# Kernel tuning notes

Hardware: AMD Instinct MI355X
Metric: run time of the kernel (lower is better)

Reference implementation:

```python
import jax, jax.numpy as jnp
import numpy as np

T, D, F, E, TOPK = 4096, 2048, 4096, 8, 2


def setup_inputs() -> dict:
    key = jax.random.key(0)
    ks = jax.random.split(key, 5)
    scale = 0.02
    return {
        "x": jax.random.normal(ks[0], (T, D), dtype=jnp.float32),
        "gate_w": jax.random.normal(ks[1], (D, E), dtype=jnp.float32) * scale,
        "w1": jax.random.normal(ks[2], (E, D, F), dtype=jnp.float32) * scale,
        "w3": jax.random.normal(ks[3], (E, D, F), dtype=jnp.float32) * scale,
        "w2": jax.random.normal(ks[4], (E, F, D), dtype=jnp.float32) * scale,
    }


def reference(x, gate_w, w1, w3, w2):
    # --- top-k gating (matches torch.topk + softmax over selected logits) ---
    gate_logits = x @ gate_w                                   # [T, E]
    top_w, sel = jax.lax.top_k(gate_logits, TOPK)              # [T, K]
    top_w = jax.nn.softmax(top_w.astype(jnp.float32), axis=1).astype(x.dtype)
    # combine weights scattered to dense [T, E]; 0 for unselected experts
    t_idx = jnp.arange(x.shape[0])[:, None]                    # [T, 1]
    cw = jnp.zeros(gate_logits.shape, x.dtype).at[t_idx, sel].add(top_w)  # [T, E]

    # --- all experts as batched GEMMs (SwiGLU FFN), combined by gate weights ---
    h = jnp.einsum('td,edf->etf', x, w1)                       # [E, T, F]
    g = jnp.einsum('td,edf->etf', x, w3)                       # [E, T, F]
    expert_out = jnp.einsum('etf,efd->etd', jax.nn.silu(h) * g, w2)  # [E, T, D]
    return jnp.einsum('te,etd->td', cw, expert_out)            # [T, D]
```

## Files before the change

### kernel.cpp

```cpp
#include <hip/hip_runtime.h>
#include <hip/hip_bf16.h>

#define T_TOK 4096
#define DDIM  2048
#define FDIM  4096
#define NEXP  8
#define MAXROWS 9216
#define MAXMT   72
#define G1_GRID (MAXMT * 64)
#define CV2_GRID 16384
#define FUSED_GRID (512 * 41)

typedef __attribute__((ext_vector_type(4))) float f32x4;
typedef __attribute__((ext_vector_type(8))) short bf16x8;

__device__ __forceinline__ unsigned short f2b(float f) {
  union { float f; unsigned u; } c; c.f = f;
  unsigned r = c.u + 0x7FFFu + ((c.u >> 16) & 1u);
  return (unsigned short)(r >> 16);
}

__device__ __forceinline__ void gload_lds16(const void* g, void* l) {
  __builtin_amdgcn_global_load_lds((__attribute__((address_space(1))) void*)(g),
                                   (__attribute__((address_space(3))) void*)(l),
                                   16, 0, 0);
}

__device__ __forceinline__ void xcd_map2d(int bid, int MT_PER, int NT, int& mt, int& nt) {
  const int xcd = bid & 7;
  const int li = bid >> 3;
  const int grp = MT_PER * 4;
  const int ng = li / grp;
  const int rem = li % grp;
  mt = xcd * MT_PER + (rem >> 2);
  nt = ng * 4 + (rem & 3);
}

__global__ void gate_topk(const float* __restrict__ x, const float* __restrict__ gw,
                          int* __restrict__ sel_e, float* __restrict__ sel_w) {
  const int t = blockIdx.x * 4 + (threadIdx.x >> 6);
  const int l = threadIdx.x & 63;
  const float* xr = x + (size_t)t * DDIM;
  float acc[8];
  #pragma unroll
  for (int e = 0; e < 8; ++e) acc[e] = 0.f;
  for (int d = l; d < DDIM; d += 64) {
    const float xv = xr[d];
    const float* g = gw + d * 8;
    #pragma unroll
    for (int e = 0; e < 8; ++e) acc[e] = fmaf(xv, g[e], acc[e]);
  }
  #pragma unroll
  for (int e = 0; e < 8; ++e) {
    float v = acc[e];
    #pragma unroll
    for (int off = 32; off; off >>= 1) v += __shfl_xor(v, off, 64);
    acc[e] = v;
  }
  if (l == 0) {
    int e0 = 0; float v0 = acc[0];
    #pragma unroll
    for (int e = 1; e < 8; ++e) if (acc[e] > v0) { v0 = acc[e]; e0 = e; }
    int e1 = -1; float v1 = -1e30f;
    #pragma unroll
    for (int e = 0; e < 8; ++e) if (e != e0 && acc[e] > v1) { v1 = acc[e]; e1 = e; }
    const float ex = __expf(v1 - v0);
    const float w0 = 1.f / (1.f + ex);
    sel_e[t * 2] = e0; sel_e[t * 2 + 1] = e1;
    sel_w[t * 2] = w0; sel_w[t * 2 + 1] = ex * w0;
  }
}

__global__ void build_lists(const int* __restrict__ sel_e, const float* __restrict__ sel_w,
                            int* __restrict__ cnt, int* __restrict__ base,
                            int* __restrict__ row_token, float* __restrict__ row_gw,
                            int* __restrict__ trow) {
  __shared__ int c[8], f[8], b[9];
  const int tid = threadIdx.x;
  if (tid < 8) { c[tid] = 0; f[tid] = 0; }
  __syncthreads();
  for (int t = tid; t < T_TOK; t += 256) {
    atomicAdd(&c[sel_e[t * 2]], 1);
    atomicAdd(&c[sel_e[t * 2 + 1]], 1);
  }
  __syncthreads();
  if (tid == 0) {
    int r = 0;
    for (int e = 0; e < 8; ++e) { b[e] = r; r += ((c[e] + 127) >> 7) << 7; }
    b[8] = r;
    for (int e = 0; e < 8; ++e) { cnt[e] = c[e]; base[e] = b[e]; }
    base[8] = r;
  }
  __syncthreads();
  for (int i = tid; i < MAXROWS; i += 256) { row_token[i] = -1; row_gw[i] = 0.f; }
  __syncthreads();
  for (int t = tid; t < T_TOK; t += 256) {
    #pragma unroll
    for (int k = 0; k < 2; ++k) {
      const int e = sel_e[t * 2 + k];
      const int p = b[e] + atomicAdd(&f[e], 1);
      row_token[p] = t; row_gw[p] = sel_w[t * 2 + k];
      trow[t * 2 + k] = p;
    }
  }
}

__global__ void gather_x(const float* __restrict__ x, const int* __restrict__ base,
                         const int* __restrict__ row_token, unsigned short* __restrict__ xc) {
  const int i = blockIdx.x;
  if (i >= base[8]) return;
  const int t = row_token[i];
  const int tid = threadIdx.x;
  union { uint4 u; unsigned short s[8]; } o;
  if (t < 0) { o.u.x = 0u; o.u.y = 0u; o.u.z = 0u; o.u.w = 0u; }
  else {
    const float4* src = (const float4*)(x + (size_t)t * DDIM + tid * 8);
    const float4 a = src[0], bb = src[1];
    o.s[0] = f2b(a.x);  o.s[1] = f2b(a.y);  o.s[2] = f2b(a.z);  o.s[3] = f2b(a.w);
    o.s[4] = f2b(bb.x); o.s[5] = f2b(bb.y); o.s[6] = f2b(bb.z); o.s[7] = f2b(bb.w);
  }
  ((uint4*)(xc + (size_t)i * DDIM))[tid] = o.u;
}

__device__ __forceinline__ void conv_tile(const float* s, unsigned short* d,
                                          int R, int C, int rowMul, int rowAdd,
                                          int r0, int c0, int tid,
                                          unsigned short (*T)[68]) {
  {
    const int i = tid >> 2, jb = (tid & 3) * 16;
    #pragma unroll
    for (int k2 = 0; k2 < 4; ++k2) {
      const float4 v = *(const float4*)(s + (size_t)(r0 + i) * C + c0 + jb + k2 * 4);
      uint2 uu;
      uu.x = (unsigned)f2b(v.x) | ((unsigned)f2b(v.y) << 16);
      uu.y = (unsigned)f2b(v.z) | ((unsigned)f2b(v.w) << 16);
      *(uint2*)&T[i][jb + k2 * 4] = uu;
    }
  }
  __syncthreads();
  {
    const int j = tid >> 2, ib = (tid & 3) * 16;
    union { uint4 q[2]; unsigned short s16[16]; } pk;
    #pragma unroll
    for (int i = 0; i < 16; ++i) pk.s16[i] = T[ib + i][j];
    unsigned short* drow = d + (size_t)(rowMul * (c0 + j) + rowAdd) * R + r0 + ib;
    *(uint4*)drow = pk.q[0];
    *(uint4*)(drow + 8) = pk.q[1];
  }
}

__global__ void conv_w13(const float* __restrict__ w1, const float* __restrict__ w3,
                         unsigned short* __restrict__ dst) {
  __shared__ unsigned short T[64][68];
  const int z = blockIdx.z;
  const int e = z & 7;
  const int isw3 = z >> 3;
  const float* s = (isw3 ? w3 : w1) + (size_t)e * DDIM * FDIM;
  unsigned short* d = dst + (size_t)e * DDIM * FDIM * 2;
  conv_tile(s, d, DDIM, FDIM, 2, isw3, blockIdx.x * 64, blockIdx.y * 64, threadIdx.x, T);
}

__global__ void conv_w2(const float* __restrict__ w2, unsigned short* __restrict__ dst) {
  __shared__ unsigned short T[64][68];
  const int e = blockIdx.z;
  const float* s = w2 + (size_t)e * FDIM * DDIM;
  unsigned short* d = dst + (size_t)e * FDIM * DDIM;
  conv_tile(s, d, FDIM, DDIM, 1, 0, blockIdx.x * 64, blockIdx.y * 64, threadIdx.x, T);
}

__device__ __forceinline__ void gemm1_body(int bid,
                                           const unsigned short* __restrict__ A,
                                           const unsigned short* __restrict__ B,
                                           const int* __restrict__ base,
                                           unsigned short* __restrict__ hid,
                                           unsigned short* As, unsigned short* Bs) {
  constexpr int KDIM = DDIM;
  constexpr int NDIM = 2 * FDIM;

  int mt, nt;
  xcd_map2d(bid, MAXMT / 8, NDIM / 128, mt, nt);

  const int m0 = mt * 128;
  if (m0 >= base[8]) return;
  int e = 0;
  #pragma unroll
  for (int qq = 1; qq < 8; ++qq) if (m0 >= base[qq]) e = qq;
  const int n0 = nt * 128;
  const unsigned short* Bp = B + (size_t)e * NDIM * KDIM;

  const int tid = threadIdx.x;
  const int l = tid & 63;
  const int w = tid >> 6;
  const int wm = w >> 1, wn = w & 1;
  const int lr = l & 15, kc = l >> 4;

  const f32x4 vzero = {0.f, 0.f, 0.f, 0.f};
  f32x4 acc[4][4];
  #pragma unroll
  for (int i = 0; i < 4; ++i)
    #pragma unroll
    for (int j = 0; j < 4; ++j) acc[i][j] = vzero;

  const int srow = w * 32 + (l >> 3);
  const int sc = l & 7;
  const unsigned short* Arow = A + (size_t)(m0 + srow) * KDIM;
  const unsigned short* Brow = Bp + (size_t)(n0 + srow) * KDIM;

  for (int k0 = 0; k0 < KDIM; k0 += 64) {
    #pragma unroll
    for (int qq = 0; qq < 4; ++qq) {
      const int r = srow + qq * 8;
      const int cg = (sc ^ (r & 7)) << 3;
      gload_lds16(Arow + (size_t)qq * 8 * KDIM + k0 + cg, As + w * 2048 + qq * 512);
      gload_lds16(Brow + (size_t)qq * 8 * KDIM + k0 + cg, Bs + w * 2048 + qq * 512);
    }
    __syncthreads();
    #pragma unroll
    for (int ks = 0; ks < 2; ++ks) {
      bf16x8 af[4], bfr[4];
      #pragma unroll
      for (int mf = 0; mf < 4; ++mf) {
        const int r = wm * 64 + mf * 16 + lr;
        const int c = (ks * 4 + kc) ^ (r & 7);
        af[mf] = *(const bf16x8*)((const char*)As + r * 128 + c * 16);
      }
      #pragma unroll
      for (int nf = 0; nf < 4; ++nf) {
        const int n = wn * 64 + nf * 16 + lr;
        const int c = (ks * 4 + kc) ^ (n & 7);
        bfr[nf] = *(const bf16x8*)((const char*)Bs + n * 128 + c * 16);
      }
      #pragma unroll
      for (int mf = 0; mf < 4; ++mf)
        #pragma unroll
        for (int nf = 0; nf < 4; ++nf)
          acc[mf][nf] = __builtin_amdgcn_mfma_f32_16x16x32_bf16(af[mf], bfr[nf], acc[mf][nf], 0, 0, 0);
    }
    __syncthreads();
  }

  const int fbase = (n0 >> 1) + wn * 32;
  #pragma unroll
  for (int mf = 0; mf < 4; ++mf) {
    const int row = m0 + wm * 64 + mf * 16 + (kc << 2);
    #pragma unroll
    for (int nf = 0; nf < 4; ++nf)
      #pragma unroll
      for (int rr = 0; rr < 4; ++rr) {
        const float v = acc[mf][nf][rr];
        const float o = __shfl_xor(v, 1, 64);
        const float h = (l & 1) ? o : v;
        const float g = (l & 1) ? v : o;
        const float res = (h / (1.f + __expf(-h))) * g;
        const float vc = __shfl(res, (l & 48) | ((l & 7) << 1), 64);
        if (lr < 8)
          hid[(size_t)(row + rr) * FDIM + fbase + nf * 8 + (l & 7)] = f2b(vc);
      }
  }
}

__global__ void moe_gemm1(const unsigned short* __restrict__ A,
                          const unsigned short* __restrict__ B,
                          const int* __restrict__ base,
                          unsigned short* __restrict__ hid) {
  __shared__ __align__(16) unsigned short As[128 * 64];
  __shared__ __align__(16) unsigned short Bs[128 * 64];
  gemm1_body(blockIdx.x, A, B, base, hid, As, Bs);
}

__global__ void gemm1_fused(const unsigned short* __restrict__ A,
                            const unsigned short* __restrict__ B,
                            const int* __restrict__ base,
                            unsigned short* __restrict__ hid,
                            const float* __restrict__ w2,
                            unsigned short* __restrict__ w2t) {
  __shared__ __align__(16) unsigned short As[128 * 64];
  __shared__ __align__(16) unsigned short Bs[128 * 64];
  const int g = blockIdx.x / 41;
  const int r = blockIdx.x % 41;
  if (r < 9) {
    gemm1_body(g * 9 + r, A, B, base, hid, As, Bs);
  } else {
    const int cid = g * 32 + (r - 9);
    const int e = cid >> 11;
    const int rem = cid & 2047;
    const int r0 = (rem >> 5) * 64;
    const int c0 = (rem & 31) * 64;
    conv_tile(w2 + (size_t)e * FDIM * DDIM, w2t + (size_t)e * FDIM * DDIM,
              FDIM, DDIM, 1, 0, r0, c0, threadIdx.x, (unsigned short (*)[68])As);
  }
}

__global__ void moe_gemm2(const unsigned short* __restrict__ A,
                          const unsigned short* __restrict__ B,
                          const int* __restrict__ base,
                          unsigned short* __restrict__ eo) {
  constexpr int KDIM = FDIM;
  constexpr int NDIM = DDIM;

  int mt, ntl;
  xcd_map2d(blockIdx.x, MAXMT / 8, NDIM / 128, mt, ntl);

  const int m0 = mt * 128;
  if (m0 >= base[8]) return;
  int e = 0;
  #pragma unroll
  for (int qq = 1; qq < 8; ++qq) if (m0 >= base[qq]) e = qq;
  const int n0 = ntl * 128;
  const unsigned short* Bp = B + (size_t)e * NDIM * KDIM;

  __shared__ __align__(16) unsigned short As[128 * 64];
  __shared__ __align__(16) unsigned short Bs[128 * 64];

  const int tid = threadIdx.x;
  const int l = tid & 63;
  const int w = tid >> 6;
  const int wm = w >> 1, wn = w & 1;
  const int lr = l & 15, kc = l >> 4;

  const f32x4 vzero = {0.f, 0.f, 0.f, 0.f};
  f32x4 acc[4][4];
  #pragma unroll
  for (int i = 0; i < 4; ++i)
    #pragma unroll
    for (int j = 0; j < 4; ++j) acc[i][j] = vzero;

  const int srow = w * 32 + (l >> 3);
  const int sc = l & 7;
  const unsigned short* Arow = A + (size_t)(m0 + srow) * KDIM;
  const unsigned short* Brow = Bp + (size_t)(n0 + srow) * KDIM;

  for (int k0 = 0; k0 < KDIM; k0 += 64) {
    #pragma unroll
    for (int qq = 0; qq < 4; ++qq) {
      const int r = srow + qq * 8;
      const int cg = (sc ^ (r & 7)) << 3;
      gload_lds16(Arow + (size_t)qq * 8 * KDIM + k0 + cg,
                  (unsigned short*)As + w * 2048 + qq * 512);
      gload_lds16(Brow + (size_t)qq * 8 * KDIM + k0 + cg,
                  (unsigned short*)Bs + w * 2048 + qq * 512);
    }
    __syncthreads();
    #pragma unroll
    for (int ks = 0; ks < 2; ++ks) {
      bf16x8 af[4], bfr[4];
      #pragma unroll
      for (int mf = 0; mf < 4; ++mf) {
        const int r = wm * 64 + mf * 16 + lr;
        const int c = (ks * 4 + kc) ^ (r & 7);
        af[mf] = *(const bf16x8*)((const char*)As + r * 128 + c * 16);
      }
      #pragma unroll
      for (int nf = 0; nf < 4; ++nf) {
        const int n = wn * 64 + nf * 16 + lr;
        const int c = (ks * 4 + kc) ^ (n & 7);
        bfr[nf] = *(const bf16x8*)((const char*)Bs + n * 128 + c * 16);
      }
      #pragma unroll
      for (int mf = 0; mf < 4; ++mf)
        #pragma unroll
        for (int nf = 0; nf < 4; ++nf)
          acc[mf][nf] = __builtin_amdgcn_mfma_f32_16x16x32_bf16(af[mf], bfr[nf], acc[mf][nf], 0, 0, 0);
    }
    __syncthreads();
  }
  #pragma unroll
  for (int mf = 0; mf < 4; ++mf) {
    const int row = m0 + wm * 64 + mf * 16 + (kc << 2);
    #pragma unroll
    for (int rr = 0; rr < 4; ++rr) {
      unsigned short* erow = eo + (size_t)(row + rr) * DDIM;
      #pragma unroll
      for (int nf = 0; nf < 4; ++nf) {
        const int col = n0 + wn * 64 + nf * 16 + lr;
        erow[col] = f2b(acc[mf][nf][rr]);
      }
    }
  }
}

__global__ void combine_k(const unsigned short* __restrict__ eo,
                          const int* __restrict__ trow, const float* __restrict__ sel_w,
                          float* __restrict__ out) {
  const int t = blockIdx.x;
  const int r0 = trow[t * 2], r1 = trow[t * 2 + 1];
  const float w0 = sel_w[t * 2], w1 = sel_w[t * 2 + 1];
  const int c = threadIdx.x * 8;
  union { uint4 u; unsigned short s[8]; } a, b;
  a.u = *(const uint4*)(eo + (size_t)r0 * DDIM + c);
  b.u = *(const uint4*)(eo + (size_t)r1 * DDIM + c);
  float o[8];
  #pragma unroll
  for (int j = 0; j < 8; ++j) {
    union { unsigned u; float f; } fa, fb;
    fa.u = (unsigned)a.s[j] << 16;
    fb.u = (unsigned)b.s[j] << 16;
    o[j] = w0 * fa.f + w1 * fb.f;
  }
  float4* dst = (float4*)(out + (size_t)t * DDIM + c);
  dst[0] = make_float4(o[0], o[1], o[2], o[3]);
  dst[1] = make_float4(o[4], o[5], o[6], o[7]);
}

#define OFF_CNT   0u
#define OFF_BASE  64u
#define OFF_SELE  4096u
#define OFF_SELW  36864u
#define OFF_RTOK  69632u
#define OFF_RGW   106496u
#define OFF_TROW  143360u
#define OFF_XC    1048576u
#define OFF_HID   38797312u
#define OFF_WBUF  114294784u
#define OFF_W2T   382730240ull
#define WS_NEED   516947968ull

extern "C" void kernel_launch(void* const* d_in, const int* in_sizes, int n_in,
                              void* d_out, int out_size, void* d_ws, size_t ws_size,
                              hipStream_t stream) {
  const float* x  = (const float*)d_in[0];
  const float* gw = (const float*)d_in[1];
  const float* w1 = (const float*)d_in[2];
  const float* w3 = (const float*)d_in[3];
  const float* w2 = (const float*)d_in[4];
  float* out = (float*)d_out;
  char* ws = (char*)d_ws;

  int*   cnt   = (int*)(ws + OFF_CNT);
  int*   base  = (int*)(ws + OFF_BASE);
  int*   sel_e = (int*)(ws + OFF_SELE);
  float* sel_w = (float*)(ws + OFF_SELW);
  int*   rtok  = (int*)(ws + OFF_RTOK);
  float* rgw   = (float*)(ws + OFF_RGW);
  int*   trow  = (int*)(ws + OFF_TROW);
  unsigned short* xc   = (unsigned short*)(ws + OFF_XC);
  unsigned short* hid  = (unsigned short*)(ws + OFF_HID);
  unsigned short* wbuf = (unsigned short*)(ws + OFF_WBUF);
  unsigned short* w2t  = (unsigned short*)(ws + OFF_W2T);
  unsigned short* eo   = xc;

  const bool fused = (ws_size >= WS_NEED);

  gate_topk<<<T_TOK / 4, 256, 0, stream>>>(x, gw, sel_e, sel_w);
  build_lists<<<1, 256, 0, stream>>>(sel_e, sel_w, cnt, base, rtok, rgw, trow);
  gather_x<<<MAXROWS, 256, 0, stream>>>(x, base, rtok, xc);
  conv_w13<<<dim3(32, 64, 16), 256, 0, stream>>>(w1, w3, wbuf);

  if (fused) {
    gemm1_fused<<<FUSED_GRID, 256, 0, stream>>>(xc, wbuf, base, hid, w2, w2t);
    moe_gemm2<<<MAXMT * 16, 256, 0, stream>>>(hid, w2t, base, eo);
  } else {
    moe_gemm1<<<G1_GRID, 256, 0, stream>>>(xc, wbuf, base, hid);
    conv_w2<<<dim3(64, 32, 8), 256, 0, stream>>>(w2, wbuf);
    moe_gemm2<<<MAXMT * 16, 256, 0, stream>>>(hid, wbuf, base, eo);
  }
  combine_k<<<T_TOK, 256, 0, stream>>>(eo, trow, sel_w, out);
}
```

Before: 778.0 us.

## Merge gather_x into conv_w13 launch and batch w2 conversion tiles per block

Fuses the x gather/bf16 conversion into the w1/w3 conversion kernel as extra blocks of one flat 1D grid, removing a kernel launch and its tail. In the fused gemm1 kernel, each w2-conversion block now processes four 64x64 tiles instead of one, so the grid shrinks from 41 to 17 blocks per group. The LDS transpose tile padding changes from 68 to 70 and the packed store becomes two 32-bit writes, aiming to cut bank conflicts. Fewer, longer conversion blocks may balance differently against the GEMM blocks.

```diff
diff --git a/kernel.cpp b/kernel.cpp
--- a/kernel.cpp
+++ b/kernel.cpp
@@ -8,8 +8,8 @@
 #define MAXROWS 9216
 #define MAXMT   72
 #define G1_GRID (MAXMT * 64)
-#define CV2_GRID 16384
-#define FUSED_GRID (512 * 41)
+#define CONV13_BLOCKS 32768
+#define FUSED_GRID (512 * 17)
 
 typedef __attribute__((ext_vector_type(4))) float f32x4;
 typedef __attribute__((ext_vector_type(8))) short bf16x8;
@@ -105,36 +105,18 @@
   }
 }
 
-__global__ void gather_x(const float* __restrict__ x, const int* __restrict__ base,
-                         const int* __restrict__ row_token, unsigned short* __restrict__ xc) {
-  const int i = blockIdx.x;
-  if (i >= base[8]) return;
-  const int t = row_token[i];
-  const int tid = threadIdx.x;
-  union { uint4 u; unsigned short s[8]; } o;
-  if (t < 0) { o.u.x = 0u; o.u.y = 0u; o.u.z = 0u; o.u.w = 0u; }
-  else {
-    const float4* src = (const float4*)(x + (size_t)t * DDIM + tid * 8);
-    const float4 a = src[0], bb = src[1];
-    o.s[0] = f2b(a.x);  o.s[1] = f2b(a.y);  o.s[2] = f2b(a.z);  o.s[3] = f2b(a.w);
-    o.s[4] = f2b(bb.x); o.s[5] = f2b(bb.y); o.s[6] = f2b(bb.z); o.s[7] = f2b(bb.w);
-  }
-  ((uint4*)(xc + (size_t)i * DDIM))[tid] = o.u;
-}
-
 __device__ __forceinline__ void conv_tile(const float* s, unsigned short* d,
                                           int R, int C, int rowMul, int rowAdd,
                                           int r0, int c0, int tid,
-                                          unsigned short (*T)[68]) {
+                                          unsigned short (*T)[70]) {
   {
     const int i = tid >> 2, jb = (tid & 3) * 16;
     #pragma unroll
     for (int k2 = 0; k2 < 4; ++k2) {
       const float4 v = *(const float4*)(s + (size_t)(r0 + i) * C + c0 + jb + k2 * 4);
-      uint2 uu;
-      uu.x = (unsigned)f2b(v.x) | ((unsigned)f2b(v.y) << 16);
-      uu.y = (unsigned)f2b(v.z) | ((unsigned)f2b(v.w) << 16);
-      *(uint2*)&T[i][jb + k2 * 4] = uu;
+      unsigned* p = (unsigned*)&T[i][jb + k2 * 4];
+      p[0] = (unsigned)f2b(v.x) | ((unsigned)f2b(v.y) << 16);
+      p[1] = (unsigned)f2b(v.z) | ((unsigned)f2b(v.w) << 16);
     }
   }
   __syncthreads();
@@ -149,19 +131,41 @@
   }
 }
 
-__global__ void conv_w13(const float* __restrict__ w1, const float* __restrict__ w3,
-                         unsigned short* __restrict__ dst) {
-  __shared__ unsigned short T[64][68];
-  const int z = blockIdx.z;
-  const int e = z & 7;
-  const int isw3 = z >> 3;
-  const float* s = (isw3 ? w3 : w1) + (size_t)e * DDIM * FDIM;
-  unsigned short* d = dst + (size_t)e * DDIM * FDIM * 2;
-  conv_tile(s, d, DDIM, FDIM, 2, isw3, blockIdx.x * 64, blockIdx.y * 64, threadIdx.x, T);
+__global__ void conv13_gather(const float* __restrict__ w1, const float* __restrict__ w3,
+                              unsigned short* __restrict__ dst,
+                              const float* __restrict__ x, const int* __restrict__ base,
+                              const int* __restrict__ row_token,
+                              unsigned short* __restrict__ xc) {
+  __shared__ unsigned short T[64][70];
+  const int bid = blockIdx.x;
+  if (bid < CONV13_BLOCKS) {
+    const int z = bid >> 11;
+    const int y = (bid >> 5) & 63;
+    const int xg = bid & 31;
+    const int e = z & 7;
+    const int isw3 = z >> 3;
+    const float* s = (isw3 ? w3 : w1) + (size_t)e * DDIM * FDIM;
+    unsigned short* d = dst + (size_t)e * DDIM * FDIM * 2;
+    conv_tile(s, d, DDIM, FDIM, 2, isw3, xg * 64, y * 64, threadIdx.x, T);
+  } else {
+    const int i = bid - CONV13_BLOCKS;
+    if (i >= base[8]) return;
+    const int t = row_token[i];
+    const int tid = threadIdx.x;
+    union { uint4 u; unsigned short s[8]; } o;
+    if (t < 0) { o.u.x = 0u; o.u.y = 0u; o.u.z = 0u; o.u.w = 0u; }
+    else {
+      const float4* src = (const float4*)(x + (size_t)t * DDIM + tid * 8);
+      const float4 a = src[0], bb = src[1];
+      o.s[0] = f2b(a.x);  o.s[1] = f2b(a.y);  o.s[2] = f2b(a.z);  o.s[3] = f2b(a.w);
+      o.s[4] = f2b(bb.x); o.s[5] = f2b(bb.y); o.s[6] = f2b(bb.z); o.s[7] = f2b(bb.w);
+    }
+    ((uint4*)(xc + (size_t)i * DDIM))[tid] = o.u;
+  }
 }
 
 __global__ void conv_w2(const float* __restrict__ w2, unsigned short* __restrict__ dst) {
-  __shared__ unsigned short T[64][68];
+  __shared__ unsigned short T[64][70];
   const int e = blockIdx.z;
   const float* s = w2 + (size_t)e * FDIM * DDIM;
   unsigned short* d = dst + (size_t)e * FDIM * DDIM;
@@ -276,18 +280,24 @@
                             unsigned short* __restrict__ w2t) {
   __shared__ __align__(16) unsigned short As[128 * 64];
   __shared__ __align__(16) unsigned short Bs[128 * 64];
-  const int g = blockIdx.x / 41;
-  const int r = blockIdx.x % 41;
+  const int g = blockIdx.x / 17;
+  const int r = blockIdx.x % 17;
   if (r < 9) {
     gemm1_body(g * 9 + r, A, B, base, hid, As, Bs);
   } else {
-    const int cid = g * 32 + (r - 9);
-    const int e = cid >> 11;
-    const int rem = cid & 2047;
-    const int r0 = (rem >> 5) * 64;
-    const int c0 = (rem & 31) * 64;
-    conv_tile(w2 + (size_t)e * FDIM * DDIM, w2t + (size_t)e * FDIM * DDIM,
-              FDIM, DDIM, 1, 0, r0, c0, threadIdx.x, (unsigned short (*)[68])As);
+    const int u = g * 8 + (r - 9);
+    unsigned short (*T)[70] = (unsigned short (*)[70])As;
+    #pragma unroll
+    for (int j = 0; j < 4; ++j) {
+      const int cid = u * 4 + j;
+      const int e = cid >> 11;
+      const int rem = cid & 2047;
+      const int r0 = (rem >> 5) * 64;
+      const int c0 = (rem & 31) * 64;
+      conv_tile(w2 + (size_t)e * FDIM * DDIM, w2t + (size_t)e * FDIM * DDIM,
+                FDIM, DDIM, 1, 0, r0, c0, threadIdx.x, T);
+      __syncthreads();
+    }
   }
 }
 
@@ -443,8 +453,8 @@
 
   gate_topk<<<T_TOK / 4, 256, 0, stream>>>(x, gw, sel_e, sel_w);
   build_lists<<<1, 256, 0, stream>>>(sel_e, sel_w, cnt, base, rtok, rgw, trow);
-  gather_x<<<MAXROWS, 256, 0, stream>>>(x, base, rtok, xc);
-  conv_w13<<<dim3(32, 64, 16), 256, 0, stream>>>(w1, w3, wbuf);
+  conv13_gather<<<CONV13_BLOCKS + MAXROWS, 256, 0, stream>>>(w1, w3, wbuf,
+                                                             x, base, rtok, xc);
 
   if (fused) {
     gemm1_fused<<<FUSED_GRID, 256, 0, stream>>>(xc, wbuf, base, hid, w2, w2t);
```

Result: no change. 771.0 us (-0.9%).
